# Kernel tuning notes

Hardware: AMD Instinct MI355X
Metric: run time of the kernel (lower is better)

Reference implementation:

```python
import jax, jax.numpy as jnp
import numpy as np

B, L, D = 32, 2048, 128
SCALE = 1.0 / float(np.sqrt(D))  # scale = 1/sqrt(dim_K) per docstring


def setup_inputs() -> dict:
    key = jax.random.key(0)
    kq, kk, kv, kb = jax.random.split(key, 4)
    return {
        "Q": jax.random.normal(kq, (B, L, D), dtype=jnp.float32),
        "K": jax.random.normal(kk, (B, L, D), dtype=jnp.float32),
        "V": jax.random.normal(kv, (B, L, D), dtype=jnp.float32),
        "bias": jax.random.normal(kb, (L, L), dtype=jnp.float32),
    }


def reference(Q, K, V, bias):
    # scores = Q @ K^T + bias (bias broadcast over batch), then scale, softmax, @ V
    scores = jnp.einsum("bqd,bkd->bqk", Q, K) + bias[None, :, :]
    attn = jax.nn.softmax(scores * SCALE, axis=-1)  # [B, L, L]
    context = jnp.einsum("bqk,bkd->bqd", attn, V)   # [B, L, D]
    return (context, attn[0])
```

## Files before the change

### kernel.cpp

```cpp
#include <hip/hip_runtime.h>
#include <cstdint>
#include <cstddef>

#define L_ 2048
#define D_ 128
#define B_ 32
#define NT_ 32

static constexpr float SCALE = 0.08838834764831845f;
static constexpr float LOG2E = 1.4426950408889634f;
static constexpr float THR_  = 8.0f;

typedef __bf16 bf16x8 __attribute__((ext_vector_type(8)));
typedef __bf16 bf16x4 __attribute__((ext_vector_type(4)));
typedef float  f32x4  __attribute__((ext_vector_type(4)));
typedef int    i32x4  __attribute__((ext_vector_type(4)));

typedef const __attribute__((address_space(1))) uint32_t* gas_t;
typedef __attribute__((address_space(3))) uint32_t*       las_t;

__device__ __forceinline__ void dma16(const void* g, void* l) {
  __builtin_amdgcn_global_load_lds((gas_t)g, (las_t)l, 16, 0, 0);
}

__device__ __forceinline__ int cperm(int r) {
  return (r & 32) | (((r >> 3) & 1) << 4) | (((r >> 2) & 1) << 3)
       | (((r >> 4) & 1) << 2) | (r & 3);
}

__global__ __launch_bounds__(256) void prep_kv(
    const float* __restrict__ K, const float* __restrict__ V,
    __bf16* __restrict__ gK, __bf16* __restrict__ gVt)
{
  const int b   = blockIdx.x >> 5;
  const int kt  = blockIdx.x & 31;
  const int tid = threadIdx.x;
  const size_t tile = ((size_t)b * NT_ + kt) * 8192;

#pragma unroll
  for (int i = 0; i < 4; ++i) {
    const int g  = tid + i * 256;
    const int r  = g >> 4;
    const int c  = g & 15;
    const int d0 = (c ^ (r & 7)) * 8;
    const float* src = K + ((size_t)b * L_ + kt * 64 + r) * D_ + d0;
    float4 a = *(const float4*)src;
    float4 e = *(const float4*)(src + 4);
    bf16x8 f;
    f[0]=(__bf16)a.x; f[1]=(__bf16)a.y; f[2]=(__bf16)a.z; f[3]=(__bf16)a.w;
    f[4]=(__bf16)e.x; f[5]=(__bf16)e.y; f[6]=(__bf16)e.z; f[7]=(__bf16)e.w;
    *(bf16x8*)((char*)(gK + tile) + r * 256 + c * 16) = f;
  }

  __shared__ alignas(16) __bf16 Vt[8192];
  char* vb = (char*)Vt;
  const int vr     = tid & 63;
  const int vc     = cperm(vr);
  const int vdbase = (tid >> 6) * 32;
  const float* vrow = V + ((size_t)b * L_ + kt * 64 + vr) * D_ + vdbase;
#pragma unroll
  for (int c = 0; c < 8; ++c) {
    float4 v4 = *(const float4*)(vrow + c * 4);
    const int d0 = vdbase + c * 4;
    float vv[4] = {v4.x, v4.y, v4.z, v4.w};
#pragma unroll
    for (int jj = 0; jj < 4; ++jj) {
      const int d = d0 + jj;
      *(__bf16*)(vb + d * 128 + ((vc * 2) ^ ((d & 7) << 4))) = (__bf16)vv[jj];
    }
  }
  __syncthreads();
#pragma unroll
  for (int i = 0; i < 4; ++i) {
    const int off = (tid + i * 256) * 16;
    *(i32x4*)((char*)(gVt + tile) + off) = *(const i32x4*)(vb + off);
  }
}

__global__ __launch_bounds__(256) void prep_bias(
    const float* __restrict__ bias, float* __restrict__ biasS)
{
#pragma unroll
  for (int it = 0; it < 4; ++it) {
    const size_t idx = ((size_t)it * 1024 + blockIdx.x) * 256 + threadIdx.x;
    float4 v = ((const float4*)bias)[idx];
    v.x *= SCALE; v.y *= SCALE; v.z *= SCALE; v.w *= SCALE;
    ((float4*)biasS)[idx] = v;
  }
}

template<int MODE>
__global__ __launch_bounds__(512, 4) void attn_fwd(
    const float* __restrict__ Q, const float* __restrict__ K,
    const float* __restrict__ V, const float* __restrict__ bias,
    const float* __restrict__ biasS,
    const __bf16* __restrict__ gK, const __bf16* __restrict__ gVt,
    float* __restrict__ ctx, float* __restrict__ attn0)
{
  const int id   = blockIdx.x;
  const int idx  = id >> 3;
  const int b    = (id & 7) * 4 + (idx >> 4);
  const int qblk = idx & 15;

  const int tid  = threadIdx.x;
  const int wave = tid >> 6;
  const int lane = tid & 63;
  const int lg   = lane >> 4;
  const int lr   = lane & 15;

  const int qbase = qblk * 128 + wave * 16;

  __shared__ alignas(16) __bf16 Ksh[2 * 8192];
  __shared__ alignas(16) __bf16 Vtsh[2 * 8192];

  bf16x8 qf[4];
  {
    const float* qrow = Q + ((size_t)b * L_ + (qbase + lr)) * D_;
#pragma unroll
    for (int kc = 0; kc < 4; ++kc) {
      const int d0 = kc * 32 + lg * 8;
      float4 a = *(const float4*)(qrow + d0);
      float4 c = *(const float4*)(qrow + d0 + 4);
      bf16x8 f;
      f[0] = (__bf16)(a.x * SCALE); f[1] = (__bf16)(a.y * SCALE);
      f[2] = (__bf16)(a.z * SCALE); f[3] = (__bf16)(a.w * SCALE);
      f[4] = (__bf16)(c.x * SCALE); f[5] = (__bf16)(c.y * SCALE);
      f[6] = (__bf16)(c.z * SCALE); f[7] = (__bf16)(c.w * SCALE);
      qf[kc] = f;
    }
  }

  f32x4 Oacc[8];
#pragma unroll
  for (int i = 0; i < 8; ++i) Oacc[i] = (f32x4){0.f, 0.f, 0.f, 0.f};
  float m_run = -3.0e38f;
  float lp    = 0.f;

  auto stage_dma = [&](int kt, int bufsel) {
    const char* gk = (const char*)(gK + ((size_t)b * NT_ + kt) * 8192);
    const char* gv = (const char*)(gVt + ((size_t)b * NT_ + kt) * 8192);
    char* kdst = (char*)Ksh + bufsel * 16384;
    char* vdst = (char*)Vtsh + bufsel * 16384;
#pragma unroll
    for (int i = 0; i < 2; ++i) {
      const int off = (wave * 2 + i) * 1024;
      dma16(gk + off + lane * 16, kdst + off);
      dma16(gv + off + lane * 16, vdst + off);
    }
  };

  if constexpr (MODE >= 1) { stage_dma(0, 0); stage_dma(1, 1); }

  for (int kt = 0; kt < NT_; ++kt) {
    const int kvbase = kt * 64;
    const int cur = (MODE >= 1) ? (kt & 1) : 0;
    const char* kb = (const char*)Ksh + cur * 16384;
    const char* vb = (const char*)Vtsh + cur * 16384;

    if constexpr (MODE >= 1) {
      if (kt + 1 < NT_) asm volatile("s_waitcnt vmcnt(4)" ::: "memory");
      else              asm volatile("s_waitcnt vmcnt(0)" ::: "memory");
      __builtin_amdgcn_s_barrier();
      __builtin_amdgcn_sched_barrier(0);
    } else {
#pragma unroll
      for (int it = 0; it < 4; ++it) {
        const int g  = tid + it * 512;
        const int r  = g >> 5;
        const int d0 = (g & 31) * 4;
        const size_t src = ((size_t)b * L_ + (kvbase + r)) * D_ + d0;
        float4 kv4 = *(const float4*)(K + src);
        bf16x4 k4 = {(__bf16)kv4.x, (__bf16)kv4.y, (__bf16)kv4.z, (__bf16)kv4.w};
        *(bf16x4*)((char*)Ksh + r * 256 + ((d0 * 2) ^ ((r & 7) << 4))) = k4;
      }
      {
        const int vr = tid & 63;
        const int vc = cperm(vr);
        const int vdbase = (tid >> 6) * 16;
        const float* vrow = V + ((size_t)b * L_ + (kvbase + vr)) * D_ + vdbase;
#pragma unroll
        for (int c = 0; c < 4; ++c) {
          float4 v4 = *(const float4*)(vrow + c * 4);
          const int d0 = vdbase + c * 4;
          float vv[4] = {v4.x, v4.y, v4.z, v4.w};
#pragma unroll
          for (int jj = 0; jj < 4; ++jj) {
            const int d = d0 + jj;
            *(__bf16*)((char*)Vtsh + d * 128 + ((vc * 2) ^ ((d & 7) << 4))) = (__bf16)vv[jj];
          }
        }
      }
      __syncthreads();
    }

    float4 bf4[4];
    {
      const float* bp = (MODE == 2 ? biasS : bias)
                        + (size_t)(qbase + lr) * L_ + kvbase + lg * 4;
#pragma unroll
      for (int t = 0; t < 4; ++t) bf4[t] = *(const float4*)(bp + t * 16);
    }

    f32x4 Sacc[4];
#pragma unroll
    for (int t = 0; t < 4; ++t) Sacc[t] = (f32x4){0.f, 0.f, 0.f, 0.f};
    __builtin_amdgcn_s_setprio(1);
#pragma unroll
    for (int t = 0; t < 4; ++t) {
      const int r   = t * 16 + lr;
      const int swz = (r & 7) << 4;
#pragma unroll
      for (int kc = 0; kc < 4; ++kc) {
        const int d0 = kc * 32 + lg * 8;
        bf16x8 kf = *(const bf16x8*)(kb + r * 256 + ((d0 * 2) ^ swz));
        Sacc[t] = __builtin_amdgcn_mfma_f32_16x16x32_bf16(kf, qf[kc], Sacc[t], 0, 0, 0);
      }
    }
    __builtin_amdgcn_s_setprio(0);

    float zz[4][4];
#pragma unroll
    for (int t = 0; t < 4; ++t) {
      if constexpr (MODE == 2) {
        zz[t][0] = Sacc[t][0] + bf4[t].x; zz[t][1] = Sacc[t][1] + bf4[t].y;
        zz[t][2] = Sacc[t][2] + bf4[t].z; zz[t][3] = Sacc[t][3] + bf4[t].w;
      } else {
        zz[t][0] = fmaf(bf4[t].x, SCALE, Sacc[t][0]);
        zz[t][1] = fmaf(bf4[t].y, SCALE, Sacc[t][1]);
        zz[t][2] = fmaf(bf4[t].z, SCALE, Sacc[t][2]);
        zz[t][3] = fmaf(bf4[t].w, SCALE, Sacc[t][3]);
      }
    }
    if (b == 0) {
      float* ap = attn0 + (size_t)(qbase + lr) * L_ + kvbase + lg * 4;
#pragma unroll
      for (int t = 0; t < 4; ++t)
        *(float4*)(ap + t * 16) = make_float4(zz[t][0], zz[t][1], zz[t][2], zz[t][3]);
    }

    float mt = fmaxf(fmaxf(fmaxf(zz[0][0], zz[0][1]), fmaxf(zz[0][2], zz[0][3])),
                     fmaxf(fmaxf(zz[1][0], zz[1][1]), fmaxf(zz[1][2], zz[1][3])));
    mt = fmaxf(mt, fmaxf(fmaxf(zz[2][0], zz[2][1]), fmaxf(zz[2][2], zz[2][3])));
    mt = fmaxf(mt, fmaxf(fmaxf(zz[3][0], zz[3][1]), fmaxf(zz[3][2], zz[3][3])));
    mt = fmaxf(mt, __shfl_xor(mt, 16));
    mt = fmaxf(mt, __shfl_xor(mt, 32));

    if (__any(mt > m_run + THR_)) {
      const float mnew = fmaxf(m_run, mt);
      const float corr = exp2f((m_run - mnew) * LOG2E);
      m_run = mnew;
      lp *= corr;
      float cR[4];
#pragma unroll
      for (int j = 0; j < 4; ++j)
        cR[j] = __shfl(corr, (lane & 0x30) | (lg * 4 + j));
#pragma unroll
      for (int dt = 0; dt < 8; ++dt) {
        Oacc[dt][0] *= cR[0]; Oacc[dt][1] *= cR[1];
        Oacc[dt][2] *= cR[2]; Oacc[dt][3] *= cR[3];
      }
    }

    bf16x4 pbf[4];
    const float mh = m_run * LOG2E;
#pragma unroll
    for (int t = 0; t < 4; ++t) {
#pragma unroll
      for (int j = 0; j < 4; ++j) {
        const float p = exp2f(fmaf(zz[t][j], LOG2E, -mh));
        lp += p;
        pbf[t][j] = (__bf16)p;
      }
    }

    __builtin_amdgcn_s_setprio(1);
#pragma unroll
    for (int kc2 = 0; kc2 < 2; ++kc2) {
      bf16x8 pa;
      pa[0] = pbf[kc2 * 2][0];     pa[1] = pbf[kc2 * 2][1];
      pa[2] = pbf[kc2 * 2][2];     pa[3] = pbf[kc2 * 2][3];
      pa[4] = pbf[kc2 * 2 + 1][0]; pa[5] = pbf[kc2 * 2 + 1][1];
      pa[6] = pbf[kc2 * 2 + 1][2]; pa[7] = pbf[kc2 * 2 + 1][3];
      const int c0 = kc2 * 32;
#pragma unroll
      for (int dt = 0; dt < 8; ++dt) {
        const int d = dt * 16 + lr;
        bf16x8 vf = *(const bf16x8*)(vb + d * 128 + (((c0 + lg * 8) * 2) ^ ((d & 7) << 4)));
        Oacc[dt] = __builtin_amdgcn_mfma_f32_16x16x32_bf16(pa, vf, Oacc[dt], 0, 0, 0);
      }
    }
    __builtin_amdgcn_s_setprio(0);

    if constexpr (MODE >= 1) {
      __builtin_amdgcn_sched_barrier(0);
      __builtin_amdgcn_s_barrier();
      __builtin_amdgcn_sched_barrier(0);
      if (kt + 2 < NT_) stage_dma(kt + 2, cur);
    } else {
      __syncthreads();
    }
  }

  float ls = lp;
  ls += __shfl_xor(ls, 16);
  ls += __shfl_xor(ls, 32);
  const float linv = 1.f / ls;
  float invR[4];
#pragma unroll
  for (int j = 0; j < 4; ++j)
    invR[j] = __shfl(linv, (lane & 0x30) | (lg * 4 + j));
#pragma unroll
  for (int dt = 0; dt < 8; ++dt) {
    const int d = dt * 16 + lr;
#pragma unroll
    for (int j = 0; j < 4; ++j) {
      const int q = qbase + lg * 4 + j;
      ctx[((size_t)b * L_ + q) * D_ + d] = Oacc[dt][j] * invR[j];
    }
  }
}

__global__ __launch_bounds__(256) void softmax_rows(float* __restrict__ attn0)
{
  const int row  = blockIdx.x;
  float* p = attn0 + (size_t)row * L_;
  const int tid  = threadIdx.x;
  const int wave = tid >> 6;
  const int lane = tid & 63;
  __shared__ float red[8];

  float4 a = ((const float4*)p)[tid];
  float4 c = ((const float4*)p)[tid + 256];
  float v[8] = {a.x, a.y, a.z, a.w, c.x, c.y, c.z, c.w};

  float mx = v[0];
#pragma unroll
  for (int i = 1; i < 8; ++i) mx = fmaxf(mx, v[i]);
#pragma unroll
  for (int msk = 1; msk < 64; msk <<= 1) mx = fmaxf(mx, __shfl_xor(mx, msk));
  if (lane == 0) red[wave] = mx;
  __syncthreads();
  mx = fmaxf(fmaxf(red[0], red[1]), fmaxf(red[2], red[3]));

  float e[8];
  float s = 0.f;
#pragma unroll
  for (int i = 0; i < 8; ++i) { e[i] = exp2f((v[i] - mx) * LOG2E); s += e[i]; }
#pragma unroll
  for (int msk = 1; msk < 64; msk <<= 1) s += __shfl_xor(s, msk);
  if (lane == 0) red[4 + wave] = s;
  __syncthreads();
  s = red[4] + red[5] + red[6] + red[7];
  const float inv = 1.f / s;

  float4 o0 = {e[0] * inv, e[1] * inv, e[2] * inv, e[3] * inv};
  float4 o1 = {e[4] * inv, e[5] * inv, e[6] * inv, e[7] * inv};
  ((float4*)p)[tid]       = o0;
  ((float4*)p)[tid + 256] = o1;
}

extern "C" void kernel_launch(void* const* d_in, const int* in_sizes, int n_in,
                              void* d_out, int out_size, void* d_ws, size_t ws_size,
                              hipStream_t stream) {
  const float* Q    = (const float*)d_in[0];
  const float* K    = (const float*)d_in[1];
  const float* V    = (const float*)d_in[2];
  const float* bias = (const float*)d_in[3];
  float* ctx   = (float*)d_out;
  float* attn0 = ctx + (size_t)B_ * L_ * D_;

  const size_t kvElems  = (size_t)B_ * L_ * D_;
  const size_t needKV   = 2 * kvElems * sizeof(__bf16);
  const size_t needAll  = needKV + (size_t)L_ * L_ * sizeof(float);

  __bf16* gK    = (__bf16*)d_ws;
  __bf16* gVt   = gK + kvElems;
  float*  biasS = (float*)(gVt + kvElems);

  if (ws_size >= needAll) {
    prep_kv<<<dim3(B_ * NT_), 256, 0, stream>>>(K, V, gK, gVt);
    prep_bias<<<dim3(1024), 256, 0, stream>>>(bias, biasS);
    attn_fwd<2><<<dim3(512), 512, 0, stream>>>(Q, K, V, bias, biasS, gK, gVt, ctx, attn0);
  } else if (ws_size >= needKV) {
    prep_kv<<<dim3(B_ * NT_), 256, 0, stream>>>(K, V, gK, gVt);
    attn_fwd<1><<<dim3(512), 512, 0, stream>>>(Q, K, V, bias, nullptr, gK, gVt, ctx, attn0);
  } else {
    attn_fwd<0><<<dim3(512), 512, 0, stream>>>(Q, K, V, bias, nullptr, nullptr, nullptr, ctx, attn0);
  }
  softmax_rows<<<L_, 256, 0, stream>>>(attn0);
}
```

Before: 157.8 us.

## Process 32 query rows per wave to reuse K/V LDS fragments

Halves the block to 4 waves, each handling two 16-row query tiles, so every K and V fragment read from LDS feeds two MFMAs instead of one. This is meant to cut LDS read traffic per MFMA and raise MFMA density per wave. Bias loads for the next tile are also issued early, alongside the DMA prefetch, with the vmcnt waits adjusted to match. The cost is roughly double the accumulator and score registers per wave, with launch bounds changed to 256 threads and a minimum of 2 blocks per CU. That may lower occupancy, and fewer waves per block means less latency hiding.

```diff
diff --git a/kernel.cpp b/kernel.cpp
--- a/kernel.cpp
+++ b/kernel.cpp
@@ -90,7 +90,7 @@
 }
 
 template<int MODE>
-__global__ __launch_bounds__(512, 4) void attn_fwd(
+__global__ __launch_bounds__(256, 2) void attn_fwd(
     const float* __restrict__ Q, const float* __restrict__ K,
     const float* __restrict__ V, const float* __restrict__ bias,
     const float* __restrict__ biasS,
@@ -108,14 +108,16 @@
   const int lg   = lane >> 4;
   const int lr   = lane & 15;
 
-  const int qbase = qblk * 128 + wave * 16;
-
-  __shared__ alignas(16) __bf16 Ksh[2 * 8192];
-  __shared__ alignas(16) __bf16 Vtsh[2 * 8192];
-
-  bf16x8 qf[4];
-  {
-    const float* qrow = Q + ((size_t)b * L_ + (qbase + lr)) * D_;
+  const int qbase = qblk * 128 + wave * 32;
+
+  constexpr int NBUF = (MODE >= 1) ? 2 : 1;
+  __shared__ alignas(16) __bf16 Ksh[NBUF * 8192];
+  __shared__ alignas(16) __bf16 Vtsh[NBUF * 8192];
+
+  bf16x8 qf0[4], qf1[4];
+#pragma unroll
+  for (int h = 0; h < 2; ++h) {
+    const float* qrow = Q + ((size_t)b * L_ + (qbase + h * 16 + lr)) * D_;
 #pragma unroll
     for (int kc = 0; kc < 4; ++kc) {
       const int d0 = kc * 32 + lg * 8;
@@ -126,15 +128,18 @@
       f[2] = (__bf16)(a.z * SCALE); f[3] = (__bf16)(a.w * SCALE);
       f[4] = (__bf16)(c.x * SCALE); f[5] = (__bf16)(c.y * SCALE);
       f[6] = (__bf16)(c.z * SCALE); f[7] = (__bf16)(c.w * SCALE);
-      qf[kc] = f;
-    }
-  }
-
-  f32x4 Oacc[8];
-#pragma unroll
-  for (int i = 0; i < 8; ++i) Oacc[i] = (f32x4){0.f, 0.f, 0.f, 0.f};
-  float m_run = -3.0e38f;
-  float lp    = 0.f;
+      if (h == 0) qf0[kc] = f; else qf1[kc] = f;
+    }
+  }
+
+  f32x4 O0[8], O1[8];
+#pragma unroll
+  for (int i = 0; i < 8; ++i) {
+    O0[i] = (f32x4){0.f, 0.f, 0.f, 0.f};
+    O1[i] = (f32x4){0.f, 0.f, 0.f, 0.f};
+  }
+  float m0 = -3.0e38f, m1 = -3.0e38f;
+  float lp0 = 0.f, lp1 = 0.f;
 
   auto stage_dma = [&](int kt, int bufsel) {
     const char* gk = (const char*)(gK + ((size_t)b * NT_ + kt) * 8192);
@@ -142,14 +147,30 @@
     char* kdst = (char*)Ksh + bufsel * 16384;
     char* vdst = (char*)Vtsh + bufsel * 16384;
 #pragma unroll
-    for (int i = 0; i < 2; ++i) {
-      const int off = (wave * 2 + i) * 1024;
+    for (int i = 0; i < 4; ++i) {
+      const int off = (wave * 4 + i) * 1024;
       dma16(gk + off + lane * 16, kdst + off);
       dma16(gv + off + lane * 16, vdst + off);
     }
   };
 
-  if constexpr (MODE >= 1) { stage_dma(0, 0); stage_dma(1, 1); }
+  const float* bbase = (MODE == 2) ? biasS : bias;
+  float4 bA[4], bB[4];
+  auto load_bias = [&](int kvbase) {
+    const float* p0 = bbase + (size_t)(qbase + lr) * L_ + kvbase + lg * 4;
+    const float* p1 = p0 + (size_t)16 * L_;
+#pragma unroll
+    for (int t = 0; t < 4; ++t) {
+      bA[t] = *(const float4*)(p0 + t * 16);
+      bB[t] = *(const float4*)(p1 + t * 16);
+    }
+  };
+
+  if constexpr (MODE >= 1) {
+    stage_dma(0, 0);
+    load_bias(0);
+    stage_dma(1, 1);
+  }
 
   for (int kt = 0; kt < NT_; ++kt) {
     const int kvbase = kt * 64;
@@ -158,14 +179,14 @@
     const char* vb = (const char*)Vtsh + cur * 16384;
 
     if constexpr (MODE >= 1) {
-      if (kt + 1 < NT_) asm volatile("s_waitcnt vmcnt(4)" ::: "memory");
-      else              asm volatile("s_waitcnt vmcnt(0)" ::: "memory");
+      if (kt < NT_ - 1) asm volatile("s_waitcnt vmcnt(16)" ::: "memory");
+      else              asm volatile("s_waitcnt vmcnt(8)" ::: "memory");
       __builtin_amdgcn_s_barrier();
       __builtin_amdgcn_sched_barrier(0);
     } else {
 #pragma unroll
-      for (int it = 0; it < 4; ++it) {
-        const int g  = tid + it * 512;
+      for (int it = 0; it < 8; ++it) {
+        const int g  = tid + it * 256;
         const int r  = g >> 5;
         const int d0 = (g & 31) * 4;
         const size_t src = ((size_t)b * L_ + (kvbase + r)) * D_ + d0;
@@ -176,10 +197,10 @@
       {
         const int vr = tid & 63;
         const int vc = cperm(vr);
-        const int vdbase = (tid >> 6) * 16;
+        const int vdbase = (tid >> 6) * 32;
         const float* vrow = V + ((size_t)b * L_ + (kvbase + vr)) * D_ + vdbase;
 #pragma unroll
-        for (int c = 0; c < 4; ++c) {
+        for (int c = 0; c < 8; ++c) {
           float4 v4 = *(const float4*)(vrow + c * 4);
           const int d0 = vdbase + c * 4;
           float vv[4] = {v4.x, v4.y, v4.z, v4.w};
@@ -191,19 +212,15 @@
         }
       }
       __syncthreads();
-    }
-
-    float4 bf4[4];
-    {
-      const float* bp = (MODE == 2 ? biasS : bias)
-                        + (size_t)(qbase + lr) * L_ + kvbase + lg * 4;
-#pragma unroll
-      for (int t = 0; t < 4; ++t) bf4[t] = *(const float4*)(bp + t * 16);
-    }
-
-    f32x4 Sacc[4];
-#pragma unroll
-    for (int t = 0; t < 4; ++t) Sacc[t] = (f32x4){0.f, 0.f, 0.f, 0.f};
+      load_bias(kvbase);
+    }
+
+    f32x4 S0[4], S1[4];
+#pragma unroll
+    for (int t = 0; t < 4; ++t) {
+      S0[t] = (f32x4){0.f, 0.f, 0.f, 0.f};
+      S1[t] = (f32x4){0.f, 0.f, 0.f, 0.f};
+    }
     __builtin_amdgcn_s_setprio(1);
 #pragma unroll
     for (int t = 0; t < 4; ++t) {
@@ -213,80 +230,96 @@
       for (int kc = 0; kc < 4; ++kc) {
         const int d0 = kc * 32 + lg * 8;
         bf16x8 kf = *(const bf16x8*)(kb + r * 256 + ((d0 * 2) ^ swz));
-        Sacc[t] = __builtin_amdgcn_mfma_f32_16x16x32_bf16(kf, qf[kc], Sacc[t], 0, 0, 0);
+        S0[t] = __builtin_amdgcn_mfma_f32_16x16x32_bf16(kf, qf0[kc], S0[t], 0, 0, 0);
+        S1[t] = __builtin_amdgcn_mfma_f32_16x16x32_bf16(kf, qf1[kc], S1[t], 0, 0, 0);
       }
     }
     __builtin_amdgcn_s_setprio(0);
 
-    float zz[4][4];
 #pragma unroll
     for (int t = 0; t < 4; ++t) {
       if constexpr (MODE == 2) {
-        zz[t][0] = Sacc[t][0] + bf4[t].x; zz[t][1] = Sacc[t][1] + bf4[t].y;
-        zz[t][2] = Sacc[t][2] + bf4[t].z; zz[t][3] = Sacc[t][3] + bf4[t].w;
+        S0[t][0] += bA[t].x; S0[t][1] += bA[t].y; S0[t][2] += bA[t].z; S0[t][3] += bA[t].w;
+        S1[t][0] += bB[t].x; S1[t][1] += bB[t].y; S1[t][2] += bB[t].z; S1[t][3] += bB[t].w;
       } else {
-        zz[t][0] = fmaf(bf4[t].x, SCALE, Sacc[t][0]);
-        zz[t][1] = fmaf(bf4[t].y, SCALE, Sacc[t][1]);
-        zz[t][2] = fmaf(bf4[t].z, SCALE, Sacc[t][2]);
-        zz[t][3] = fmaf(bf4[t].w, SCALE, Sacc[t][3]);
+        S0[t][0] = fmaf(bA[t].x, SCALE, S0[t][0]); S0[t][1] = fmaf(bA[t].y, SCALE, S0[t][1]);
+        S0[t][2] = fmaf(bA[t].z, SCALE, S0[t][2]); S0[t][3] = fmaf(bA[t].w, SCALE, S0[t][3]);
+        S1[t][0] = fmaf(bB[t].x, SCALE, S1[t][0]); S1[t][1] = fmaf(bB[t].y, SCALE, S1[t][1]);
+        S1[t][2] = fmaf(bB[t].z, SCALE, S1[t][2]); S1[t][3] = fmaf(bB[t].w, SCALE, S1[t][3]);
       }
     }
     if (b == 0) {
-      float* ap = attn0 + (size_t)(qbase + lr) * L_ + kvbase + lg * 4;
-#pragma unroll
-      for (int t = 0; t < 4; ++t)
-        *(float4*)(ap + t * 16) = make_float4(zz[t][0], zz[t][1], zz[t][2], zz[t][3]);
-    }
-
-    float mt = fmaxf(fmaxf(fmaxf(zz[0][0], zz[0][1]), fmaxf(zz[0][2], zz[0][3])),
-                     fmaxf(fmaxf(zz[1][0], zz[1][1]), fmaxf(zz[1][2], zz[1][3])));
-    mt = fmaxf(mt, fmaxf(fmaxf(zz[2][0], zz[2][1]), fmaxf(zz[2][2], zz[2][3])));
-    mt = fmaxf(mt, fmaxf(fmaxf(zz[3][0], zz[3][1]), fmaxf(zz[3][2], zz[3][3])));
-    mt = fmaxf(mt, __shfl_xor(mt, 16));
-    mt = fmaxf(mt, __shfl_xor(mt, 32));
-
-    if (__any(mt > m_run + THR_)) {
-      const float mnew = fmaxf(m_run, mt);
-      const float corr = exp2f((m_run - mnew) * LOG2E);
-      m_run = mnew;
-      lp *= corr;
-      float cR[4];
-#pragma unroll
-      for (int j = 0; j < 4; ++j)
-        cR[j] = __shfl(corr, (lane & 0x30) | (lg * 4 + j));
+      float* a0 = attn0 + (size_t)(qbase + lr) * L_ + kvbase + lg * 4;
+      float* a1 = a0 + (size_t)16 * L_;
+#pragma unroll
+      for (int t = 0; t < 4; ++t) {
+        *(float4*)(a0 + t * 16) = make_float4(S0[t][0], S0[t][1], S0[t][2], S0[t][3]);
+        *(float4*)(a1 + t * 16) = make_float4(S1[t][0], S1[t][1], S1[t][2], S1[t][3]);
+      }
+    }
+
+    float mt0 = fmaxf(fmaxf(fmaxf(S0[0][0], S0[0][1]), fmaxf(S0[0][2], S0[0][3])),
+                      fmaxf(fmaxf(S0[1][0], S0[1][1]), fmaxf(S0[1][2], S0[1][3])));
+    mt0 = fmaxf(mt0, fmaxf(fmaxf(S0[2][0], S0[2][1]), fmaxf(S0[2][2], S0[2][3])));
+    mt0 = fmaxf(mt0, fmaxf(fmaxf(S0[3][0], S0[3][1]), fmaxf(S0[3][2], S0[3][3])));
+    mt0 = fmaxf(mt0, __shfl_xor(mt0, 16));
+    mt0 = fmaxf(mt0, __shfl_xor(mt0, 32));
+    float mt1 = fmaxf(fmaxf(fmaxf(S1[0][0], S1[0][1]), fmaxf(S1[0][2], S1[0][3])),
+                      fmaxf(fmaxf(S1[1][0], S1[1][1]), fmaxf(S1[1][2], S1[1][3])));
+    mt1 = fmaxf(mt1, fmaxf(fmaxf(S1[2][0], S1[2][1]), fmaxf(S1[2][2], S1[2][3])));
+    mt1 = fmaxf(mt1, fmaxf(fmaxf(S1[3][0], S1[3][1]), fmaxf(S1[3][2], S1[3][3])));
+    mt1 = fmaxf(mt1, __shfl_xor(mt1, 16));
+    mt1 = fmaxf(mt1, __shfl_xor(mt1, 32));
+
+    if (__any((mt0 > m0 + THR_) || (mt1 > m1 + THR_))) {
+      const float n0 = fmaxf(m0, mt0), c0 = exp2f((m0 - n0) * LOG2E);
+      const float n1 = fmaxf(m1, mt1), c1 = exp2f((m1 - n1) * LOG2E);
+      m0 = n0; m1 = n1; lp0 *= c0; lp1 *= c1;
+      float cR0[4], cR1[4];
+#pragma unroll
+      for (int j = 0; j < 4; ++j) {
+        cR0[j] = __shfl(c0, (lane & 0x30) | (lg * 4 + j));
+        cR1[j] = __shfl(c1, (lane & 0x30) | (lg * 4 + j));
+      }
 #pragma unroll
       for (int dt = 0; dt < 8; ++dt) {
-        Oacc[dt][0] *= cR[0]; Oacc[dt][1] *= cR[1];
-        Oacc[dt][2] *= cR[2]; Oacc[dt][3] *= cR[3];
-      }
-    }
-
-    bf16x4 pbf[4];
-    const float mh = m_run * LOG2E;
+        O0[dt][0] *= cR0[0]; O0[dt][1] *= cR0[1]; O0[dt][2] *= cR0[2]; O0[dt][3] *= cR0[3];
+        O1[dt][0] *= cR1[0]; O1[dt][1] *= cR1[1]; O1[dt][2] *= cR1[2]; O1[dt][3] *= cR1[3];
+      }
+    }
+
+    bf16x4 pb0[4], pb1[4];
+    const float mh0 = m0 * LOG2E, mh1 = m1 * LOG2E;
 #pragma unroll
     for (int t = 0; t < 4; ++t) {
 #pragma unroll
       for (int j = 0; j < 4; ++j) {
-        const float p = exp2f(fmaf(zz[t][j], LOG2E, -mh));
-        lp += p;
-        pbf[t][j] = (__bf16)p;
+        const float p0 = exp2f(fmaf(S0[t][j], LOG2E, -mh0));
+        const float p1 = exp2f(fmaf(S1[t][j], LOG2E, -mh1));
+        lp0 += p0; lp1 += p1;
+        pb0[t][j] = (__bf16)p0; pb1[t][j] = (__bf16)p1;
       }
     }
 
     __builtin_amdgcn_s_setprio(1);
 #pragma unroll
     for (int kc2 = 0; kc2 < 2; ++kc2) {
-      bf16x8 pa;
-      pa[0] = pbf[kc2 * 2][0];     pa[1] = pbf[kc2 * 2][1];
-      pa[2] = pbf[kc2 * 2][2];     pa[3] = pbf[kc2 * 2][3];
-      pa[4] = pbf[kc2 * 2 + 1][0]; pa[5] = pbf[kc2 * 2 + 1][1];
-      pa[6] = pbf[kc2 * 2 + 1][2]; pa[7] = pbf[kc2 * 2 + 1][3];
+      bf16x8 pa0, pa1;
+      pa0[0] = pb0[kc2*2][0];   pa0[1] = pb0[kc2*2][1];
+      pa0[2] = pb0[kc2*2][2];   pa0[3] = pb0[kc2*2][3];
+      pa0[4] = pb0[kc2*2+1][0]; pa0[5] = pb0[kc2*2+1][1];
+      pa0[6] = pb0[kc2*2+1][2]; pa0[7] = pb0[kc2*2+1][3];
+      pa1[0] = pb1[kc2*2][0];   pa1[1] = pb1[kc2*2][1];
+      pa1[2] = pb1[kc2*2][2];   pa1[3] = pb1[kc2*2][3];
+      pa1[4] = pb1[kc2*2+1][0]; pa1[5] = pb1[kc2*2+1][1];
+      pa1[6] = pb1[kc2*2+1][2]; pa1[7] = pb1[kc2*2+1][3];
       const int c0 = kc2 * 32;
 #pragma unroll
       for (int dt = 0; dt < 8; ++dt) {
         const int d = dt * 16 + lr;
         bf16x8 vf = *(const bf16x8*)(vb + d * 128 + (((c0 + lg * 8) * 2) ^ ((d & 7) << 4)));
-        Oacc[dt] = __builtin_amdgcn_mfma_f32_16x16x32_bf16(pa, vf, Oacc[dt], 0, 0, 0);
+        O0[dt] = __builtin_amdgcn_mfma_f32_16x16x32_bf16(pa0, vf, O0[dt], 0, 0, 0);
+        O1[dt] = __builtin_amdgcn_mfma_f32_16x16x32_bf16(pa1, vf, O1[dt], 0, 0, 0);
       }
     }
     __builtin_amdgcn_s_setprio(0);
@@ -295,27 +328,34 @@
       __builtin_amdgcn_sched_barrier(0);
       __builtin_amdgcn_s_barrier();
       __builtin_amdgcn_sched_barrier(0);
+      if (kt + 1 < NT_) load_bias((kt + 1) * 64);
       if (kt + 2 < NT_) stage_dma(kt + 2, cur);
     } else {
       __syncthreads();
     }
   }
 
-  float ls = lp;
-  ls += __shfl_xor(ls, 16);
-  ls += __shfl_xor(ls, 32);
-  const float linv = 1.f / ls;
-  float invR[4];
-#pragma unroll
-  for (int j = 0; j < 4; ++j)
-    invR[j] = __shfl(linv, (lane & 0x30) | (lg * 4 + j));
+  float ls0 = lp0;
+  ls0 += __shfl_xor(ls0, 16);
+  ls0 += __shfl_xor(ls0, 32);
+  float ls1 = lp1;
+  ls1 += __shfl_xor(ls1, 16);
+  ls1 += __shfl_xor(ls1, 32);
+  const float li0 = 1.f / ls0, li1 = 1.f / ls1;
+  float iR0[4], iR1[4];
+#pragma unroll
+  for (int j = 0; j < 4; ++j) {
+    iR0[j] = __shfl(li0, (lane & 0x30) | (lg * 4 + j));
+    iR1[j] = __shfl(li1, (lane & 0x30) | (lg * 4 + j));
+  }
 #pragma unroll
   for (int dt = 0; dt < 8; ++dt) {
     const int d = dt * 16 + lr;
 #pragma unroll
     for (int j = 0; j < 4; ++j) {
-      const int q = qbase + lg * 4 + j;
-      ctx[((size_t)b * L_ + q) * D_ + d] = Oacc[dt][j] * invR[j];
+      const int q0 = qbase + lg * 4 + j;
+      ctx[((size_t)b * L_ + q0) * D_ + d]      = O0[dt][j] * iR0[j];
+      ctx[((size_t)b * L_ + q0 + 16) * D_ + d] = O1[dt][j] * iR1[j];
     }
   }
 }
@@ -380,12 +420,12 @@
   if (ws_size >= needAll) {
     prep_kv<<<dim3(B_ * NT_), 256, 0, stream>>>(K, V, gK, gVt);
     prep_bias<<<dim3(1024), 256, 0, stream>>>(bias, biasS);
-    attn_fwd<2><<<dim3(512), 512, 0, stream>>>(Q, K, V, bias, biasS, gK, gVt, ctx, attn0);
+    attn_fwd<2><<<dim3(512), 256, 0, stream>>>(Q, K, V, bias, biasS, gK, gVt, ctx, attn0);
   } else if (ws_size >= needKV) {
     prep_kv<<<dim3(B_ * NT_), 256, 0, stream>>>(K, V, gK, gVt);
-    attn_fwd<1><<<dim3(512), 512, 0, stream>>>(Q, K, V, bias, nullptr, gK, gVt, ctx, attn0);
+    attn_fwd<1><<<dim3(512), 256, 0, stream>>>(Q, K, V, bias, nullptr, gK, gVt, ctx, attn0);
   } else {
-    attn_fwd<0><<<dim3(512), 512, 0, stream>>>(Q, K, V, bias, nullptr, nullptr, nullptr, ctx, attn0);
+    attn_fwd<0><<<dim3(512), 256, 0, stream>>>(Q, K, V, bias, nullptr, nullptr, nullptr, ctx, attn0);
   }
   softmax_rows<<<L_, 256, 0, stream>>>(attn0);
 }
```

After: 169.2 us. 1.07x slower.

## Fuse attn0 softmax normalization into attention kernel and prefetch bias

Applied to the files above, without the earlier changes.

Removes the separate prep_bias and softmax_rows kernels. Batch-0 blocks now normalize their own attn0 rows at the end, reusing the running max and row sum they already hold. The bias tile for the next step is prefetched into registers alongside the K/V DMA, with the vmcnt waits adjusted to match, and the pre-scaled bias is replaced by an fma with SCALE. The block-to-batch mapping changes to b = id>>4, which alters how batch-0 blocks, and their extra normalization work, are spread across CUs. The risk is a tail effect, since batch-0 blocks now re-read and rewrite their attn rows while the other blocks finish.

```diff
diff --git a/kernel.cpp b/kernel.cpp
--- a/kernel.cpp
+++ b/kernel.cpp
@@ -77,30 +77,16 @@
   }
 }
 
-__global__ __launch_bounds__(256) void prep_bias(
-    const float* __restrict__ bias, float* __restrict__ biasS)
-{
-#pragma unroll
-  for (int it = 0; it < 4; ++it) {
-    const size_t idx = ((size_t)it * 1024 + blockIdx.x) * 256 + threadIdx.x;
-    float4 v = ((const float4*)bias)[idx];
-    v.x *= SCALE; v.y *= SCALE; v.z *= SCALE; v.w *= SCALE;
-    ((float4*)biasS)[idx] = v;
-  }
-}
-
 template<int MODE>
 __global__ __launch_bounds__(512, 4) void attn_fwd(
     const float* __restrict__ Q, const float* __restrict__ K,
     const float* __restrict__ V, const float* __restrict__ bias,
-    const float* __restrict__ biasS,
     const __bf16* __restrict__ gK, const __bf16* __restrict__ gVt,
     float* __restrict__ ctx, float* __restrict__ attn0)
 {
   const int id   = blockIdx.x;
-  const int idx  = id >> 3;
-  const int b    = (id & 7) * 4 + (idx >> 4);
-  const int qblk = idx & 15;
+  const int b    = id >> 4;
+  const int qblk = id & 15;
 
   const int tid  = threadIdx.x;
   const int wave = tid >> 6;
@@ -149,7 +135,18 @@
     }
   };
 
-  if constexpr (MODE >= 1) { stage_dma(0, 0); stage_dma(1, 1); }
+  float4 bf4[4];
+  auto load_bias = [&](int kvbase) {
+    const float* bp = bias + (size_t)(qbase + lr) * L_ + kvbase + lg * 4;
+#pragma unroll
+    for (int t = 0; t < 4; ++t) bf4[t] = *(const float4*)(bp + t * 16);
+  };
+
+  if constexpr (MODE >= 1) {
+    stage_dma(0, 0);
+    load_bias(0);
+    stage_dma(1, 1);
+  }
 
   for (int kt = 0; kt < NT_; ++kt) {
     const int kvbase = kt * 64;
@@ -158,8 +155,8 @@
     const char* vb = (const char*)Vtsh + cur * 16384;
 
     if constexpr (MODE >= 1) {
-      if (kt + 1 < NT_) asm volatile("s_waitcnt vmcnt(4)" ::: "memory");
-      else              asm volatile("s_waitcnt vmcnt(0)" ::: "memory");
+      if (kt < NT_ - 1) asm volatile("s_waitcnt vmcnt(8)" ::: "memory");
+      else              asm volatile("s_waitcnt vmcnt(4)" ::: "memory");
       __builtin_amdgcn_s_barrier();
       __builtin_amdgcn_sched_barrier(0);
     } else {
@@ -191,14 +188,7 @@
         }
       }
       __syncthreads();
-    }
-
-    float4 bf4[4];
-    {
-      const float* bp = (MODE == 2 ? biasS : bias)
-                        + (size_t)(qbase + lr) * L_ + kvbase + lg * 4;
-#pragma unroll
-      for (int t = 0; t < 4; ++t) bf4[t] = *(const float4*)(bp + t * 16);
+      load_bias(kvbase);
     }
 
     f32x4 Sacc[4];
@@ -221,15 +211,10 @@
     float zz[4][4];
 #pragma unroll
     for (int t = 0; t < 4; ++t) {
-      if constexpr (MODE == 2) {
-        zz[t][0] = Sacc[t][0] + bf4[t].x; zz[t][1] = Sacc[t][1] + bf4[t].y;
-        zz[t][2] = Sacc[t][2] + bf4[t].z; zz[t][3] = Sacc[t][3] + bf4[t].w;
-      } else {
-        zz[t][0] = fmaf(bf4[t].x, SCALE, Sacc[t][0]);
-        zz[t][1] = fmaf(bf4[t].y, SCALE, Sacc[t][1]);
-        zz[t][2] = fmaf(bf4[t].z, SCALE, Sacc[t][2]);
-        zz[t][3] = fmaf(bf4[t].w, SCALE, Sacc[t][3]);
-      }
+      zz[t][0] = fmaf(bf4[t].x, SCALE, Sacc[t][0]);
+      zz[t][1] = fmaf(bf4[t].y, SCALE, Sacc[t][1]);
+      zz[t][2] = fmaf(bf4[t].z, SCALE, Sacc[t][2]);
+      zz[t][3] = fmaf(bf4[t].w, SCALE, Sacc[t][3]);
     }
     if (b == 0) {
       float* ap = attn0 + (size_t)(qbase + lr) * L_ + kvbase + lg * 4;
@@ -295,6 +280,7 @@
       __builtin_amdgcn_sched_barrier(0);
       __builtin_amdgcn_s_barrier();
       __builtin_amdgcn_sched_barrier(0);
+      if (kt + 1 < NT_) load_bias((kt + 1) * 64);
       if (kt + 2 < NT_) stage_dma(kt + 2, cur);
     } else {
       __syncthreads();
@@ -318,45 +304,24 @@
       ctx[((size_t)b * L_ + q) * D_ + d] = Oacc[dt][j] * invR[j];
     }
   }
-}
-
-__global__ __launch_bounds__(256) void softmax_rows(float* __restrict__ attn0)
-{
-  const int row  = blockIdx.x;
-  float* p = attn0 + (size_t)row * L_;
-  const int tid  = threadIdx.x;
-  const int wave = tid >> 6;
-  const int lane = tid & 63;
-  __shared__ float red[8];
-
-  float4 a = ((const float4*)p)[tid];
-  float4 c = ((const float4*)p)[tid + 256];
-  float v[8] = {a.x, a.y, a.z, a.w, c.x, c.y, c.z, c.w};
-
-  float mx = v[0];
-#pragma unroll
-  for (int i = 1; i < 8; ++i) mx = fmaxf(mx, v[i]);
-#pragma unroll
-  for (int msk = 1; msk < 64; msk <<= 1) mx = fmaxf(mx, __shfl_xor(mx, msk));
-  if (lane == 0) red[wave] = mx;
-  __syncthreads();
-  mx = fmaxf(fmaxf(red[0], red[1]), fmaxf(red[2], red[3]));
-
-  float e[8];
-  float s = 0.f;
-#pragma unroll
-  for (int i = 0; i < 8; ++i) { e[i] = exp2f((v[i] - mx) * LOG2E); s += e[i]; }
-#pragma unroll
-  for (int msk = 1; msk < 64; msk <<= 1) s += __shfl_xor(s, msk);
-  if (lane == 0) red[4 + wave] = s;
-  __syncthreads();
-  s = red[4] + red[5] + red[6] + red[7];
-  const float inv = 1.f / s;
-
-  float4 o0 = {e[0] * inv, e[1] * inv, e[2] * inv, e[3] * inv};
-  float4 o1 = {e[4] * inv, e[5] * inv, e[6] * inv, e[7] * inv};
-  ((float4*)p)[tid]       = o0;
-  ((float4*)p)[tid + 256] = o1;
+
+  if (b == 0) {
+#pragma unroll 1
+    for (int rr = 0; rr < 16; ++rr) {
+      const float mr = __shfl(m_run, rr) * LOG2E;
+      const float iv = __shfl(linv, rr);
+      float4* rowp = (float4*)(attn0 + (size_t)(qbase + rr) * L_);
+#pragma unroll
+      for (int c = 0; c < 8; ++c) {
+        float4 v = rowp[c * 64 + lane];
+        v.x = exp2f(fmaf(v.x, LOG2E, -mr)) * iv;
+        v.y = exp2f(fmaf(v.y, LOG2E, -mr)) * iv;
+        v.z = exp2f(fmaf(v.z, LOG2E, -mr)) * iv;
+        v.w = exp2f(fmaf(v.w, LOG2E, -mr)) * iv;
+        rowp[c * 64 + lane] = v;
+      }
+    }
+  }
 }
 
 extern "C" void kernel_launch(void* const* d_in, const int* in_sizes, int n_in,
@@ -369,23 +334,16 @@
   float* ctx   = (float*)d_out;
   float* attn0 = ctx + (size_t)B_ * L_ * D_;
 
-  const size_t kvElems  = (size_t)B_ * L_ * D_;
-  const size_t needKV   = 2 * kvElems * sizeof(__bf16);
-  const size_t needAll  = needKV + (size_t)L_ * L_ * sizeof(float);
-
-  __bf16* gK    = (__bf16*)d_ws;
-  __bf16* gVt   = gK + kvElems;
-  float*  biasS = (float*)(gVt + kvElems);
-
-  if (ws_size >= needAll) {
+  const size_t kvElems = (size_t)B_ * L_ * D_;
+  const size_t needKV  = 2 * kvElems * sizeof(__bf16);
+
+  __bf16* gK  = (__bf16*)d_ws;
+  __bf16* gVt = gK + kvElems;
+
+  if (ws_size >= needKV) {
     prep_kv<<<dim3(B_ * NT_), 256, 0, stream>>>(K, V, gK, gVt);
-    prep_bias<<<dim3(1024), 256, 0, stream>>>(bias, biasS);
-    attn_fwd<2><<<dim3(512), 512, 0, stream>>>(Q, K, V, bias, biasS, gK, gVt, ctx, attn0);
-  } else if (ws_size >= needKV) {
-    prep_kv<<<dim3(B_ * NT_), 256, 0, stream>>>(K, V, gK, gVt);
-    attn_fwd<1><<<dim3(512), 512, 0, stream>>>(Q, K, V, bias, nullptr, gK, gVt, ctx, attn0);
+    attn_fwd<1><<<dim3(512), 512, 0, stream>>>(Q, K, V, bias, gK, gVt, ctx, attn0);
   } else {
-    attn_fwd<0><<<dim3(512), 512, 0, stream>>>(Q, K, V, bias, nullptr, nullptr, nullptr, ctx, attn0);
-  }
-  softmax_rows<<<L_, 256, 0, stream>>>(attn0);
-}
+    attn_fwd<0><<<dim3(512), 512, 0, stream>>>(Q, K, V, bias, nullptr, nullptr, ctx, attn0);
+  }
+}
```

Result: slower. 167.8 us (+6.4%).
